# Optimization experiments

Hardware: AMD Instinct MI355X
Metric: run time of the kernel (lower is better)

Reference implementation:

```python
import jax, jax.numpy as jnp
import numpy as np

QUERY_DIM = 256
HIDDEN_DIM = 256
NUM_HEADS = 8
HEAD_DIM = HIDDEN_DIM // NUM_HEADS
NORM_FACT = float(HIDDEN_DIM / NUM_HEADS) ** (-0.5)


def setup_inputs() -> dict:
    key = jax.random.key(0)
    ks = jax.random.split(key, 7)
    b, Q, H, W = 4, 300, 100, 100
    q = jax.random.normal(ks[0], (b, Q, QUERY_DIM), dtype=jnp.float32)
    k = jax.random.normal(ks[1], (b, QUERY_DIM, H, W), dtype=jnp.float32)
    mask = jax.random.randint(ks[2], (b, H, W), 0, 2).astype(jnp.bool_)
    # xavier_uniform for Linear(query_dim, hidden_dim): bound = sqrt(6/(fan_in+fan_out))
    bound = float(np.sqrt(6.0 / (QUERY_DIM + HIDDEN_DIM)))
    q_w = jax.random.uniform(ks[3], (HIDDEN_DIM, QUERY_DIM), jnp.float32, -bound, bound)
    k_w = jax.random.uniform(ks[4], (HIDDEN_DIM, QUERY_DIM), jnp.float32, -bound, bound)
    q_b = jnp.zeros((HIDDEN_DIM,), jnp.float32)
    k_b = jnp.zeros((HIDDEN_DIM,), jnp.float32)
    return {"q": q, "k": k, "mask": mask, "q_w": q_w, "q_b": q_b, "k_w": k_w, "k_b": k_b}


def reference(q, k, mask, q_w, q_b, k_w, k_b):
    b, Q, _ = q.shape
    _, C, H, W = k.shape
    # q_linear: [b,Q,query_dim] -> [b,Q,hidden]
    qp = jnp.einsum('bqc,hc->bqh', q, q_w) + q_b
    # k projection: 1x1 conv == channel-wise linear: [b,C,H,W] -> [b,hidden,H,W]
    kp = jnp.einsum('bchw,oc->bohw', k, k_w) + k_b[None, :, None, None]
    qh = qp.reshape(b, Q, NUM_HEADS, HEAD_DIM)
    kh = kp.reshape(b, NUM_HEADS, HEAD_DIM, H, W)
    # attention scores: [b, Q, n_heads, H, W]
    weights = jnp.einsum('bqnc,bnchw->bqnhw', qh * NORM_FACT, kh)
    if mask is not None:
        weights = jnp.where(mask[:, None, None, :, :], -jnp.inf, weights)
    # softmax over flattened (heads, H, W) — faithful to flatten(2) in the original
    flat = weights.reshape(b, Q, NUM_HEADS * H * W)
    weights = jax.nn.softmax(flat, axis=-1).reshape(b, Q, NUM_HEADS, H, W)
    return weights
```

## Files before the change

### kernel.cpp

```cpp
#include <hip/hip_runtime.h>
#include <math.h>

#define BB 4
#define QQ 300
#define CC 256
#define NH 8
#define HD 32
#define HWN 10000
#define NT 625
#define NCHUNK 125
#define TPC 5
#define MT 19
#define NORM_FACT 0.17677669529663687f

typedef __attribute__((ext_vector_type(8))) short short8_t;
typedef __attribute__((ext_vector_type(4))) float f32x4_t;
typedef __attribute__((ext_vector_type(4))) int   i32x4_t;

union FragU { uint32_t u[4]; short8_t v; };

__device__ __forceinline__ unsigned short bf16_rn(float x) {
    uint32_t u = __float_as_uint(x);
    return (unsigned short)((u + 0x7fffu + ((u >> 16) & 1u)) >> 16);
}
__device__ __forceinline__ float bf16_f(unsigned short h) {
    return __uint_as_float(((uint32_t)h) << 16);
}

__global__ void prep_kwB_kernel(const float* __restrict__ kw,
                                unsigned short* __restrict__ kwB_hi,
                                unsigned short* __restrict__ kwB_lo) {
    const int ot = blockIdx.x, ks = blockIdx.y;
    const int l = threadIdx.x;
    const int o = ot * 16 + (l & 15);
    const int c0 = ks * 32 + (l >> 4) * 8;
    const size_t base = ((size_t)(ot * 8 + ks) * 64 + l) * 8;
    #pragma unroll
    for (int j = 0; j < 8; ++j) {
        const float x = kw[o * CC + c0 + j];
        const unsigned short h = bf16_rn(x);
        kwB_hi[base + j] = h;
        kwB_lo[base + j] = bf16_rn(x - bf16_f(h));
    }
}

__global__ void qproj_kernel(const float* __restrict__ q,
                             const float* __restrict__ qw,
                             const float* __restrict__ qb,
                             unsigned short* __restrict__ qp_il) {
    __shared__ float qrow[CC];
    const int bq = blockIdx.x;
    const int h  = threadIdx.x;
    qrow[h] = q[bq * CC + h];
    __syncthreads();
    float acc = qb[h];
    const float* wr = qw + h * CC;
    #pragma unroll 4
    for (int c = 0; c < CC; c += 4) {
        float4 w = *reinterpret_cast<const float4*>(wr + c);
        float4 x = *reinterpret_cast<const float4*>(&qrow[c]);
        acc += w.x * x.x + w.y * x.y + w.z * x.z + w.w * x.w;
    }
    acc *= NORM_FACT;
    const unsigned short hi = bf16_rn(acc);
    const size_t base = ((size_t)bq * NH + (h >> 5)) * 64 + (h & 31);
    qp_il[base]      = hi;
    qp_il[base + 32] = bf16_rn(acc - bf16_f(hi));
}

__global__ __launch_bounds__(256)
void kproj_kernel(const float* __restrict__ kin,
                  const unsigned short* __restrict__ kwB_hi,
                  const unsigned short* __restrict__ kwB_lo,
                  const float* __restrict__ kb,
                  unsigned short* __restrict__ kp_il) {
    __shared__ float kf[CC][17];
    const int wid = threadIdx.x >> 6, l = threadIdx.x & 63;
    const int bu  = blockIdx.x;
    const int hwt = bu % NT;
    const int b   = bu / NT;
    const int ot4 = wid;

    {
        const int tid = threadIdx.x;
        const float* kb0 = kin + (size_t)b * CC * HWN + hwt * 16;
        #pragma unroll
        for (int iter = 0; iter < 4; ++iter) {
            const int c   = iter * 64 + (tid >> 2);
            const int col = (tid & 3) * 4;
            const float4 v = *reinterpret_cast<const float4*>(
                kb0 + (size_t)c * HWN + col);
            kf[c][col]     = v.x;
            kf[c][col + 1] = v.y;
            kf[c][col + 2] = v.z;
            kf[c][col + 3] = v.w;
        }
    }
    __syncthreads();

    const int jb  = (l >> 4) * 8;
    const int col = l & 15;

    f32x4_t acc[4];
    #pragma unroll
    for (int t = 0; t < 4; ++t) {
        const float bias = kb[(ot4 * 4 + t) * 16 + col];
        acc[t] = {bias, bias, bias, bias};
    }

    #pragma unroll 2
    for (int ks = 0; ks < 8; ++ks) {
        FragU a_hi, a_lo;
        #pragma unroll
        for (int tt = 0; tt < 4; ++tt) {
            const int c = ks * 32 + jb + 2 * tt;
            const float x0 = kf[c][col];
            const float x1 = kf[c + 1][col];
            const unsigned short h0 = bf16_rn(x0), h1 = bf16_rn(x1);
            const unsigned short g0 = bf16_rn(x0 - bf16_f(h0));
            const unsigned short g1 = bf16_rn(x1 - bf16_f(h1));
            a_hi.u[tt] = (uint32_t)h0 | ((uint32_t)h1 << 16);
            a_lo.u[tt] = (uint32_t)g0 | ((uint32_t)g1 << 16);
        }
        #pragma unroll
        for (int t = 0; t < 4; ++t) {
            const int ot = ot4 * 4 + t;
            const size_t fb = ((size_t)(ot * 8 + ks) * 64 + l) * 8;
            const short8_t bh = *reinterpret_cast<const short8_t*>(kwB_hi + fb);
            const short8_t bl = *reinterpret_cast<const short8_t*>(kwB_lo + fb);
            acc[t] = __builtin_amdgcn_mfma_f32_16x16x32_bf16(a_hi.v, bh, acc[t], 0, 0, 0);
            acc[t] = __builtin_amdgcn_mfma_f32_16x16x32_bf16(a_hi.v, bl, acc[t], 0, 0, 0);
            acc[t] = __builtin_amdgcn_mfma_f32_16x16x32_bf16(a_lo.v, bh, acc[t], 0, 0, 0);
        }
    }

    #pragma unroll
    for (int t = 0; t < 4; ++t) {
        const int o = (ot4 * 4 + t) * 16 + col;
        const int n = o >> 5, osub = o & 31;
        #pragma unroll
        for (int r = 0; r < 4; ++r) {
            const int hwrow = hwt * 16 + (l >> 4) * 4 + r;
            const size_t base = ((size_t)(b * HWN + hwrow) * NH + n) * 64 + osub;
            const float v = acc[t][r];
            const unsigned short h = bf16_rn(v);
            kp_il[base]      = h;
            kp_il[base + 32] = bf16_rn(v - bf16_f(h));
        }
    }
}

__global__ __launch_bounds__(256)
void attn_stats_kernel(const unsigned short* __restrict__ qp_il,
                       const unsigned short* __restrict__ kp_il,
                       const int* __restrict__ mask,
                       float* __restrict__ partials) {
    const int wid = threadIdx.x >> 6, l = threadIdx.x & 63;
    const int wu = blockIdx.x * 4 + wid;
    const int qh = wu & 1;
    int tmp = wu >> 1;
    const int ch = tmp % NCHUNK; tmp /= NCHUNK;
    const int n = tmp & 7;
    const int b = tmp >> 3;

    short8_t ah[TPC], al[TPC];
    float mf[TPC][4];
    #pragma unroll
    for (int t = 0; t < TPC; ++t) {
        const int tile = ch * TPC + t;
        const int hwr = tile * 16 + (l & 15);
        const size_t abase = ((size_t)(b * HWN + hwr) * NH + n) * 64 + (l >> 4) * 8;
        ah[t] = *reinterpret_cast<const short8_t*>(kp_il + abase);
        al[t] = *reinterpret_cast<const short8_t*>(kp_il + abase + 32);
        const int hw4 = tile * 16 + (l >> 4) * 4;
        const i32x4_t mv = *reinterpret_cast<const i32x4_t*>(mask + b * HWN + hw4);
        mf[t][0] = mv.x ? 0.f : 1.f;
        mf[t][1] = mv.y ? 0.f : 1.f;
        mf[t][2] = mv.z ? 0.f : 1.f;
        mf[t][3] = mv.w ? 0.f : 1.f;
    }

    const int qt0 = qh * 10;
    const int qt1 = qh ? MT : 10;
    #pragma unroll 2
    for (int qt = qt0; qt < qt1; ++qt) {
        const int qa = qt * 16 + (l & 15);
        const int qcl = qa < QQ ? qa : QQ - 1;
        const size_t bbase = ((size_t)(b * QQ + qcl) * NH + n) * 64 + (l >> 4) * 8;
        const short8_t bh = *reinterpret_cast<const short8_t*>(qp_il + bbase);
        const short8_t bl = *reinterpret_cast<const short8_t*>(qp_il + bbase + 32);

        float a = 0.f;
        #pragma unroll
        for (int t = 0; t < TPC; ++t) {
            f32x4_t c = {0.f, 0.f, 0.f, 0.f};
            c = __builtin_amdgcn_mfma_f32_16x16x32_bf16(ah[t], bh, c, 0, 0, 0);
            c = __builtin_amdgcn_mfma_f32_16x16x32_bf16(ah[t], bl, c, 0, 0, 0);
            c = __builtin_amdgcn_mfma_f32_16x16x32_bf16(al[t], bh, c, 0, 0, 0);
            a += __expf(c[0]) * mf[t][0] + __expf(c[1]) * mf[t][1]
               + __expf(c[2]) * mf[t][2] + __expf(c[3]) * mf[t][3];
        }
        a += __shfl_xor(a, 16, 64);
        a += __shfl_xor(a, 32, 64);
        if (l < 16) {
            const int qr = qt * 16 + l;
            if (qr < QQ)
                partials[(((size_t)b * QQ + qr) * NH + n) * NCHUNK + ch] = a;
        }
    }
}

__global__ void invsum_kernel(const float* __restrict__ partials,
                              float* __restrict__ invS) {
    const int row = blockIdx.x;
    const int l = threadIdx.x;
    float s = 0.f;
    const float* p = partials + (size_t)row * (NH * NCHUNK);
    for (int i = l; i < NH * NCHUNK; i += 64) s += p[i];
    #pragma unroll
    for (int m = 1; m < 64; m <<= 1) s += __shfl_xor(s, m, 64);
    if (l == 0) invS[row] = 1.0f / s;
}

__global__ __launch_bounds__(256)
void attn_out_kernel(const unsigned short* __restrict__ qp_il,
                     const unsigned short* __restrict__ kp_il,
                     const int* __restrict__ mask,
                     const float* __restrict__ invS,
                     float* __restrict__ out) {
    const int wid = threadIdx.x >> 6, l = threadIdx.x & 63;
    const int wu = blockIdx.x * 4 + wid;
    const int qh = wu & 1;
    int tmp = wu >> 1;
    const int ch = tmp % NCHUNK; tmp /= NCHUNK;
    const int n = tmp & 7;
    const int b = tmp >> 3;

    short8_t ah[TPC], al[TPC];
    float mf[TPC][4];
    int hw4v[TPC];
    #pragma unroll
    for (int t = 0; t < TPC; ++t) {
        const int tile = ch * TPC + t;
        const int hwr = tile * 16 + (l & 15);
        const size_t abase = ((size_t)(b * HWN + hwr) * NH + n) * 64 + (l >> 4) * 8;
        ah[t] = *reinterpret_cast<const short8_t*>(kp_il + abase);
        al[t] = *reinterpret_cast<const short8_t*>(kp_il + abase + 32);
        const int hw4 = tile * 16 + (l >> 4) * 4;
        hw4v[t] = hw4;
        const i32x4_t mv = *reinterpret_cast<const i32x4_t*>(mask + b * HWN + hw4);
        mf[t][0] = mv.x ? 0.f : 1.f;
        mf[t][1] = mv.y ? 0.f : 1.f;
        mf[t][2] = mv.z ? 0.f : 1.f;
        mf[t][3] = mv.w ? 0.f : 1.f;
    }

    const int qt0 = qh * 10;
    const int qt1 = qh ? MT : 10;
    #pragma unroll 2
    for (int qt = qt0; qt < qt1; ++qt) {
        const int qa = qt * 16 + (l & 15);
        const int qcl = qa < QQ ? qa : QQ - 1;
        const bool qok = qa < QQ;
        const size_t bbase = ((size_t)(b * QQ + qcl) * NH + n) * 64 + (l >> 4) * 8;
        const short8_t bh = *reinterpret_cast<const short8_t*>(qp_il + bbase);
        const short8_t bl = *reinterpret_cast<const short8_t*>(qp_il + bbase + 32);
        const float is = invS[b * QQ + qcl];
        float* const obase = out + (((size_t)b * QQ + qcl) * NH + n) * HWN;

        #pragma unroll
        for (int t = 0; t < TPC; ++t) {
            f32x4_t c = {0.f, 0.f, 0.f, 0.f};
            c = __builtin_amdgcn_mfma_f32_16x16x32_bf16(ah[t], bh, c, 0, 0, 0);
            c = __builtin_amdgcn_mfma_f32_16x16x32_bf16(ah[t], bl, c, 0, 0, 0);
            c = __builtin_amdgcn_mfma_f32_16x16x32_bf16(al[t], bh, c, 0, 0, 0);
            f32x4_t rv;
            rv[0] = __expf(c[0]) * is * mf[t][0];
            rv[1] = __expf(c[1]) * is * mf[t][1];
            rv[2] = __expf(c[2]) * is * mf[t][2];
            rv[3] = __expf(c[3]) * is * mf[t][3];
            if (qok)
                __builtin_nontemporal_store(rv,
                    reinterpret_cast<f32x4_t*>(obase + hw4v[t]));
        }
    }
}

extern "C" void kernel_launch(void* const* d_in, const int* in_sizes, int n_in,
                              void* d_out, int out_size, void* d_ws, size_t ws_size,
                              hipStream_t stream) {
    const float* q    = (const float*)d_in[0];
    const float* k    = (const float*)d_in[1];
    const int*   mask = (const int*)d_in[2];
    const float* qw   = (const float*)d_in[3];
    const float* qb   = (const float*)d_in[4];
    const float* kw   = (const float*)d_in[5];
    const float* kb   = (const float*)d_in[6];
    float* out = (float*)d_out;

    char* wsb = (char*)d_ws;
    unsigned short* kp_il = (unsigned short*)wsb;
    unsigned short* qp_il = (unsigned short*)(wsb + 40960000);
    float* invS           = (float*)(wsb + 40960000 + 1228800);

    unsigned short* kwB_hi = (unsigned short*)d_out;
    unsigned short* kwB_lo = kwB_hi + 65536;
    float* partials = (float*)((char*)d_out + (4u << 20));

    prep_kwB_kernel<<<dim3(16, 8), 64, 0, stream>>>(kw, kwB_hi, kwB_lo);
    qproj_kernel<<<BB * QQ, 256, 0, stream>>>(q, qw, qb, qp_il);
    kproj_kernel<<<BB * NT, 256, 0, stream>>>(k, kwB_hi, kwB_lo, kb, kp_il);
    attn_stats_kernel<<<(BB * NH * NCHUNK * 2) / 4, 256, 0, stream>>>(
        qp_il, kp_il, mask, partials);
    invsum_kernel<<<BB * QQ, 64, 0, stream>>>(partials, invS);
    attn_out_kernel<<<(BB * NH * NCHUNK * 2) / 4, 256, 0, stream>>>(
        qp_il, kp_il, mask, invS, out);
}
```

Measured before the change: 251.6 us.

## Move Q projection to split-bf16 MFMA and use regular output stores

Replaces the scalar FP32 Q projection, one block per query row, with an MFMA kernel. It uses a hi/lo bf16 split of the inputs and of the pre-swizzled weights (three MFMAs per step), processes 16 rows per block, and launches 75 blocks. A second prep launch swizzles q_w into scratch space inside the output buffer. Separately, the final output store switches from nontemporal to ordinary stores, which changes cache behavior on the large 38MB output write. The Q projection is a tiny part of total time, and the store change could help or hurt.

```diff
diff --git a/kernel.cpp b/kernel.cpp
--- a/kernel.cpp
+++ b/kernel.cpp
@@ -44,28 +44,61 @@
     }
 }
 
-__global__ void qproj_kernel(const float* __restrict__ q,
-                             const float* __restrict__ qw,
-                             const float* __restrict__ qb,
-                             unsigned short* __restrict__ qp_il) {
-    __shared__ float qrow[CC];
-    const int bq = blockIdx.x;
-    const int h  = threadIdx.x;
-    qrow[h] = q[bq * CC + h];
-    __syncthreads();
-    float acc = qb[h];
-    const float* wr = qw + h * CC;
-    #pragma unroll 4
-    for (int c = 0; c < CC; c += 4) {
-        float4 w = *reinterpret_cast<const float4*>(wr + c);
-        float4 x = *reinterpret_cast<const float4*>(&qrow[c]);
-        acc += w.x * x.x + w.y * x.y + w.z * x.z + w.w * x.w;
-    }
-    acc *= NORM_FACT;
-    const unsigned short hi = bf16_rn(acc);
-    const size_t base = ((size_t)bq * NH + (h >> 5)) * 64 + (h & 31);
-    qp_il[base]      = hi;
-    qp_il[base + 32] = bf16_rn(acc - bf16_f(hi));
+__global__ __launch_bounds__(256)
+void qproj_kernel(const float* __restrict__ qin,
+                  const unsigned short* __restrict__ qwB_hi,
+                  const unsigned short* __restrict__ qwB_lo,
+                  const float* __restrict__ qb,
+                  unsigned short* __restrict__ qp_il) {
+    const int wid = threadIdx.x >> 6, l = threadIdx.x & 63;
+    const int rt = blockIdx.x;
+    const int ot4 = wid;
+    const int jb = (l >> 4) * 8;
+    const int col = l & 15;
+
+    FragU a_hi[8], a_lo[8];
+    const float* abase = qin + ((size_t)rt * 16 + col) * CC;
+    #pragma unroll
+    for (int ks = 0; ks < 8; ++ks) {
+        #pragma unroll
+        for (int tt = 0; tt < 4; ++tt) {
+            const int c = ks * 32 + jb + 2 * tt;
+            const float x0 = abase[c];
+            const float x1 = abase[c + 1];
+            const unsigned short h0 = bf16_rn(x0), h1 = bf16_rn(x1);
+            const unsigned short g0 = bf16_rn(x0 - bf16_f(h0));
+            const unsigned short g1 = bf16_rn(x1 - bf16_f(h1));
+            a_hi[ks].u[tt] = (uint32_t)h0 | ((uint32_t)h1 << 16);
+            a_lo[ks].u[tt] = (uint32_t)g0 | ((uint32_t)g1 << 16);
+        }
+    }
+
+    #pragma unroll 1
+    for (int t = 0; t < 4; ++t) {
+        const int ot = ot4 * 4 + t;
+        f32x4_t c = {0.f, 0.f, 0.f, 0.f};
+        #pragma unroll
+        for (int ks = 0; ks < 8; ++ks) {
+            const size_t fb = ((size_t)(ot * 8 + ks) * 64 + l) * 8;
+            const short8_t bh = *reinterpret_cast<const short8_t*>(qwB_hi + fb);
+            const short8_t bl = *reinterpret_cast<const short8_t*>(qwB_lo + fb);
+            c = __builtin_amdgcn_mfma_f32_16x16x32_bf16(a_hi[ks].v, bh, c, 0, 0, 0);
+            c = __builtin_amdgcn_mfma_f32_16x16x32_bf16(a_hi[ks].v, bl, c, 0, 0, 0);
+            c = __builtin_amdgcn_mfma_f32_16x16x32_bf16(a_lo[ks].v, bh, c, 0, 0, 0);
+        }
+        const int o = ot * 16 + col;
+        const int n = o >> 5, osub = o & 31;
+        const float bias = qb[o];
+        #pragma unroll
+        for (int r = 0; r < 4; ++r) {
+            const int row = rt * 16 + (l >> 4) * 4 + r;
+            const float v = (c[r] + bias) * NORM_FACT;
+            const size_t base = ((size_t)row * NH + n) * 64 + osub;
+            const unsigned short h = bf16_rn(v);
+            qp_il[base]      = h;
+            qp_il[base + 32] = bf16_rn(v - bf16_f(h));
+        }
+    }
 }
 
 __global__ __launch_bounds__(256)
@@ -87,13 +120,13 @@
         #pragma unroll
         for (int iter = 0; iter < 4; ++iter) {
             const int c   = iter * 64 + (tid >> 2);
-            const int col = (tid & 3) * 4;
+            const int cl  = (tid & 3) * 4;
             const float4 v = *reinterpret_cast<const float4*>(
-                kb0 + (size_t)c * HWN + col);
-            kf[c][col]     = v.x;
-            kf[c][col + 1] = v.y;
-            kf[c][col + 2] = v.z;
-            kf[c][col + 3] = v.w;
+                kb0 + (size_t)c * HWN + cl);
+            kf[c][cl]     = v.x;
+            kf[c][cl + 1] = v.y;
+            kf[c][cl + 2] = v.z;
+            kf[c][cl + 3] = v.w;
         }
     }
     __syncthreads();
@@ -280,8 +313,7 @@
             rv[2] = __expf(c[2]) * is * mf[t][2];
             rv[3] = __expf(c[3]) * is * mf[t][3];
             if (qok)
-                __builtin_nontemporal_store(rv,
-                    reinterpret_cast<f32x4_t*>(obase + hw4v[t]));
+                *reinterpret_cast<f32x4_t*>(obase + hw4v[t]) = rv;
         }
     }
 }
@@ -305,10 +337,13 @@
 
     unsigned short* kwB_hi = (unsigned short*)d_out;
     unsigned short* kwB_lo = kwB_hi + 65536;
+    unsigned short* qwB_hi = kwB_hi + 131072;
+    unsigned short* qwB_lo = kwB_hi + 196608;
     float* partials = (float*)((char*)d_out + (4u << 20));
 
     prep_kwB_kernel<<<dim3(16, 8), 64, 0, stream>>>(kw, kwB_hi, kwB_lo);
-    qproj_kernel<<<BB * QQ, 256, 0, stream>>>(q, qw, qb, qp_il);
+    prep_kwB_kernel<<<dim3(16, 8), 64, 0, stream>>>(qw, qwB_hi, qwB_lo);
+    qproj_kernel<<<75, 256, 0, stream>>>(q, qwB_hi, qwB_lo, qb, qp_il);
     kproj_kernel<<<BB * NT, 256, 0, stream>>>(k, kwB_hi, kwB_lo, kb, kp_il);
     attn_stats_kernel<<<(BB * NH * NCHUNK * 2) / 4, 256, 0, stream>>>(
         qp_il, kp_il, mask, partials);
```

Result: faster. 224.3 us (-10.8%).
